# Kernel tuning notes

Measured on AMD Instinct MI355X. Metric: run time of the kernel, lower is better.

The kernel has to match this reference:

```python
import jax, jax.numpy as jnp
import numpy as np

N_QUBITS = 12
DIM = 2 ** N_QUBITS
N_RES_LAYERS = 3
N_HEADS = 2
N_ATTN_LAYERS = 2
SEQ_LEN = 64
HORIZON = 4
BATCH = 8
N_PARAMS = N_QUBITS * 2 * N_ATTN_LAYERS  # 48
FEAT = N_QUBITS * N_HEADS  # 24

# ---- static (numpy) precomputed gate structures (little-endian, qiskit convention) ----
_idx = np.arange(DIM)

def _cx_perm(c, t):
    # CNOT: flip target bit where control bit is 1 -> index permutation
    return np.where(((_idx >> c) & 1) == 1, _idx ^ (1 << t), _idx)

def _cz_phase(a, b):
    return (1.0 - 2.0 * (((_idx >> a) & 1) * ((_idx >> b) & 1))).astype(np.float32)

CX_LADDER = [jnp.asarray(_cx_perm(i, i + 1)) for i in range(N_QUBITS - 1)]
CX_RING = jnp.asarray(_cx_perm(N_QUBITS - 1, 0))
CX_LONG = jnp.asarray(_cx_perm(0, N_QUBITS - 1))
_CZ = []
for _layer in range(N_RES_LAYERS):
    _ph = np.ones(DIM, np.float32)
    for _i in range(_layer % 2, N_QUBITS - 1, 2):
        _ph *= _cz_phase(_i, _i + 1)
    _CZ.append(jnp.asarray(_ph))
# Qiskit Pauli label 'I'*i + 'Z' + 'I'*(n-i-1) acts on qubit n-1-i (big-endian labels)
Z_SIGNS = jnp.asarray(np.stack([
    (1.0 - 2.0 * ((_idx >> (N_QUBITS - 1 - i)) & 1)).astype(np.float32)
    for i in range(N_QUBITS)]))  # (n, DIM)


def _apply_1q(state, gate, q):
    # state: (..., DIM); gate: (2,2) or (...,2,2) broadcastable against leading dims
    hi = DIM >> (q + 1)
    lo = 1 << q
    s = state.reshape(state.shape[:-1] + (hi, 2, lo))
    out = jnp.einsum('...ij,...hjl->...hil', gate, s)
    return out.reshape(state.shape)


def _ry(theta):
    c = jnp.cos(theta / 2)
    s = jnp.sin(theta / 2)
    g = jnp.stack([jnp.stack([c, -s], -1), jnp.stack([s, c], -1)], -2)
    return g.astype(jnp.complex64)


def _rz(phi):
    em = jnp.exp(-0.5j * phi)
    ep = jnp.exp(0.5j * phi)
    z = jnp.zeros_like(em)
    return jnp.stack([jnp.stack([em, z], -1), jnp.stack([z, ep], -1)], -2)


def _u3(t, p, l):
    ct = jnp.cos(t / 2).astype(jnp.complex64)
    st = jnp.sin(t / 2).astype(jnp.complex64)
    return jnp.stack([jnp.stack([ct, -jnp.exp(1j * l) * st]),
                      jnp.stack([jnp.exp(1j * p) * st, jnp.exp(1j * (p + l)) * ct])])


def _encode_reservoir(x, res_params):
    # x: (B,T) normalized scalars -> batched statevectors (B,T,DIM)
    B, T = x.shape
    # H^{\otimes n} |0...0> = uniform superposition
    state = jnp.full((B, T, DIM), 1.0 / np.sqrt(DIM), jnp.complex64)
    for i in range(N_QUBITS):
        state = _apply_1q(state, _ry(x * np.pi * (i + 1) / N_QUBITS), i)
        state = _apply_1q(state, _rz(x * np.pi / (i + 1)), i)
    for p in CX_LADDER:
        state = state[..., p]
    state = state[..., CX_RING]
    # fixed random reservoir
    for layer in range(N_RES_LAYERS):
        for i in range(N_QUBITS):
            g = _u3(res_params[layer, i, 0], res_params[layer, i, 1], res_params[layer, i, 2])
            state = _apply_1q(state, g, i)
        state = state * _CZ[layer]
        state = state[..., CX_LONG]  # n > 2
    return state


def _project(state, params):
    # projection circuit: per layer RY/RZ on each qubit then CNOT ladder; then <Z_i>
    for layer in range(N_ATTN_LAYERS):
        for i in range(N_QUBITS):
            k = (layer * N_QUBITS + i) * 2
            state = _apply_1q(state, _ry(params[k]), i)
            state = _apply_1q(state, _rz(params[k + 1]), i)
        for p in CX_LADDER:
            state = state[..., p]
    probs = state.real ** 2 + state.imag ** 2  # (B,T,DIM)
    return jnp.einsum('btd,qd->btq', probs, Z_SIGNS)  # (B,T,n)


def setup_inputs() -> dict:
    key = jax.random.key(0)
    ks = jax.random.split(key, 6)
    sequence = jax.random.uniform(ks[0], (BATCH, SEQ_LEN), jnp.float32)
    res_params = jax.random.uniform(ks[1], (N_RES_LAYERS, N_QUBITS, 3), jnp.float32,
                                    minval=0.0, maxval=2.0 * np.pi)
    head_params = jax.random.uniform(ks[2], (N_HEADS, 3, N_PARAMS), jnp.float32,
                                     minval=0.0, maxval=2.0 * np.pi)
    W1 = jax.random.normal(ks[3], (FEAT, 2 * FEAT), jnp.float32) / np.sqrt(FEAT)
    b1 = jnp.zeros((2 * FEAT,), jnp.float32)
    W2 = jax.random.normal(ks[4], (2 * FEAT, HORIZON), jnp.float32) / np.sqrt(2 * FEAT)
    b2 = jnp.zeros((HORIZON,), jnp.float32)
    return {'sequence': sequence, 'res_params': res_params, 'head_params': head_params,
            'W1': W1, 'b1': b1, 'W2': W2, 'b2': b2}


def reference(sequence, res_params, head_params, W1, b1, W2, b2):
    states = _encode_reservoir(sequence, res_params)  # (B,T,DIM)
    T = sequence.shape[1]
    mask = jnp.triu(jnp.full((T, T), -1e9, jnp.float32), k=1)
    outs = []
    for h in range(N_HEADS):
        Q = _project(states, head_params[h, 0])
        K = _project(states, head_params[h, 1])
        V = _project(states, head_params[h, 2])
        scores = jnp.einsum('btd,bsd->bts', Q, K) / np.sqrt(N_QUBITS) + mask
        attn = jax.nn.softmax(scores, axis=-1)
        outs.append(jnp.einsum('bts,bsd->btd', attn, V))
    feats = jnp.concatenate(outs, -1)  # (B,T,FEAT)
    last = feats[:, -1, :]
    hdn = jax.nn.gelu(last @ W1 + b1, approximate=False)  # torch GELU default = exact erf
    pred = hdn @ W2 + b2  # (B, HORIZON)
    return pred
```

## Files before the change

### kernel.cpp

```cpp
#include <hip/hip_runtime.h>
#include <hip/hip_bf16.h>


#define PADDED 4224

__device__ __forceinline__ int PD(int j) { return j + (j >> 5); }

__device__ __forceinline__ int mapIdx(int j, int mode) {
  if (mode == 1) { int k = j ^ ((j >> 11) & 1); return k ^ ((k & 0x7FF) << 1); }
  if (mode == 2) { return j ^ ((j & 1) << 11); }
  if (mode == 3) { return j ^ ((j & 0x7FF) << 1); }
  return j;
}

template <int L>
__device__ __forceinline__ int layoutIdx(int tid, int r) {
  if constexpr (L == 0) return (tid << 4) | r;
  else if constexpr (L == 1) return ((tid & 0xF0) << 4) | (r << 4) | (tid & 15);
  else return (r << 8) | tid;
}

template <int L>
__device__ __forceinline__ void ldsRead16(const float* sR, const float* sI, int tid, int mode,
                                          float ar[16], float ai[16]) {
#pragma unroll
  for (int r = 0; r < 16; ++r) {
    int j = layoutIdx<L>(tid, r);
    int a = PD(mapIdx(j, mode));
    ar[r] = sR[a]; ai[r] = sI[a];
  }
}

template <int L>
__device__ __forceinline__ void ldsWrite16(float* sR, float* sI, int tid,
                                           const float ar[16], const float ai[16], int czmask) {
#pragma unroll
  for (int r = 0; r < 16; ++r) {
    int j = layoutIdx<L>(tid, r);
    float vr = ar[r], vi = ai[r];
    if (czmask) {
      float sg = (__popc((j & (j >> 1)) & czmask) & 1) ? -1.0f : 1.0f;
      vr *= sg; vi *= sg;
    }
    int a = PD(j);
    sR[a] = vr; sI[a] = vi;
  }
}

__device__ __forceinline__ void applyU34(float ar[16], float ai[16], const float (*ut)[8]) {
#pragma unroll
  for (int b = 0; b < 4; ++b) {
    const float* u = ut[b];
    float u00r = u[0];
    float u01r = u[2], u01i = u[3];
    float u10r = u[4], u10i = u[5], u11r = u[6], u11i = u[7];
#pragma unroll
    for (int m = 0; m < 8; ++m) {
      int p0 = ((m >> b) << (b + 1)) | (m & ((1 << b) - 1));
      int p1 = p0 | (1 << b);
      float x0r = ar[p0], x0i = ai[p0], x1r = ar[p1], x1i = ai[p1];
      ar[p0] = u00r * x0r + u01r * x1r - u01i * x1i;
      ai[p0] = u00r * x0i + u01r * x1i + u01i * x1r;
      ar[p1] = u10r * x0r - u10i * x0i + u11r * x1r - u11i * x1i;
      ai[p1] = u10r * x0i + u10i * x0r + u11r * x1i + u11i * x1r;
    }
  }
}

__device__ __forceinline__ void applyRyRz4(float ar[16], float ai[16], const float4* gt) {
#pragma unroll
  for (int b = 0; b < 4; ++b) {
    float4 g = gt[b];
    float c = g.x, s = g.y, zr = g.z, zi = g.w;
#pragma unroll
    for (int m = 0; m < 8; ++m) {
      int p0 = ((m >> b) << (b + 1)) | (m & ((1 << b) - 1));
      int p1 = p0 | (1 << b);
      float x0r = ar[p0], x0i = ai[p0], x1r = ar[p1], x1i = ai[p1];
      float n0r = c * x0r - s * x1r;
      float n0i = c * x0i - s * x1i;
      float wr  = s * x0r + c * x1r;
      float wi  = s * x0i + c * x1i;
      ar[p0] = n0r;              ai[p0] = n0i;
      ar[p1] = wr * zr - wi * zi; ai[p1] = wr * zi + wi * zr;
    }
  }
}

template <int L>
__device__ __forceinline__ void encPass(float* sR, float* sI, int tid, int mode,
                                        const float (*ut)[8], int czmask) {
  float ar[16], ai[16];
  ldsRead16<L>(sR, sI, tid, mode, ar, ai);
  if (mode != 0) __syncthreads();
  applyU34(ar, ai, ut);
  ldsWrite16<L>(sR, sI, tid, ar, ai, czmask);
  __syncthreads();
}

template <int L>
__device__ __forceinline__ void projPass(float* sR, float* sI, int tid, int mode, const float4* gt) {
  float ar[16], ai[16];
  ldsRead16<L>(sR, sI, tid, mode, ar, ai);
  if (mode != 0) __syncthreads();
  applyRyRz4(ar, ai, gt);
  ldsWrite16<L>(sR, sI, tid, ar, ai, 0);
  __syncthreads();
}

__device__ __forceinline__ void projFinal(const float* sR, const float* sI, int tid,
                                          const float4* gt, float feat[12]) {
  float ar[16], ai[16];
#pragma unroll
  for (int r = 0; r < 16; ++r) {
    int a = PD((r << 8) | tid);
    ar[r] = sR[a]; ai[r] = sI[a];
  }
  applyRyRz4(ar, ai, gt);
  float sp = 0.f, f0 = 0.f, f1 = 0.f, f2 = 0.f, f3 = 0.f;
  int pt = __popc(tid) & 1;
#pragma unroll
  for (int r = 0; r < 16; ++r) {
    float p = ar[r] * ar[r] + ai[r] * ai[r];
    sp += p;
    int tr = r ^ (r << 1); tr ^= (tr << 2);
    f0 += ((pt ^ ((tr >> 3) & 1)) ? -p : p);
    f1 += ((pt ^ ((tr >> 2) & 1)) ? -p : p);
    f2 += ((pt ^ ((tr >> 1) & 1)) ? -p : p);
    f3 += ((pt ^ (tr & 1)) ? -p : p);
  }
  feat[0] = f0; feat[1] = f1; feat[2] = f2; feat[3] = f3;
  int tt = tid ^ (tid << 1); tt ^= (tt << 2); tt ^= (tt << 4);
#pragma unroll
  for (int q = 4; q < 12; ++q)
    feat[q] = ((tt >> (11 - q)) & 1) ? -sp : sp;
}

__device__ __forceinline__ float waveReduce(float v) {
#pragma unroll
  for (int off = 32; off; off >>= 1) v += __shfl_xor(v, off, 64);
  return v;
}


__device__ __forceinline__ void buildQtab(float4* qtab, int tid, float x) {
  const float PI = 3.14159265358979323846f;
  const float RS2 = 0.70710678118654752440f;
  if (tid < 12) {
    int i = tid;
    float th = x * PI * (float)(i + 1) / 12.0f;
    float ph = x * PI / (float)(i + 1);
    float s, c;  sincosf(0.5f * th, &s, &c);
    float zi, zr; sincosf(0.5f * ph, &zi, &zr);
    float k0 = (c - s) * RS2, k1 = (c + s) * RS2;
    qtab[i] = make_float4(k0 * zr, -k0 * zi, k1 * zr, k1 * zi);
  }
}

__device__ __forceinline__ void buildUtab(float (*utab)[8], int tid, const float* resp) {
  if (tid >= 64 && tid < 100) {
    int i = tid - 64;
    const float* rp = resp + i * 3;
    float st, ct;  sincosf(0.5f * rp[0], &st, &ct);
    float sp2, cp; sincosf(rp[1], &sp2, &cp);
    float sl, cl;  sincosf(rp[2], &sl, &cl);
    float spl, cpl; sincosf(rp[1] + rp[2], &spl, &cpl);
    float* u = utab[i];
    u[0] = ct;       u[1] = 0.0f;
    u[2] = -cl * st; u[3] = -sl * st;
    u[4] = cp * st;  u[5] = sp2 * st;
    u[6] = cpl * ct; u[7] = spl * ct;
  }
}

__device__ __forceinline__ void initProduct(float* sRe, float* sIm, int tid, const float4* qtab) {
  float pr, pi;
  {
    float4 g = qtab[4];
    int sb = tid & 1;
    pr = sb ? g.z : g.x; pi = sb ? g.w : g.y;
  }
#pragma unroll
  for (int q = 5; q < 12; ++q) {
    float4 g = qtab[q];
    int sb = (tid >> (q - 4)) & 1;
    float fr = sb ? g.z : g.x, fi = sb ? g.w : g.y;
    float nr = pr * fr - pi * fi;
    pi = pr * fi + pi * fr; pr = nr;
  }
  float4 g0 = qtab[0], g1 = qtab[1], g2 = qtab[2], g3 = qtab[3];
  float c01r[4], c01i[4], c23r[4], c23i[4];
#pragma unroll
  for (int i2 = 0; i2 < 4; ++i2) {
    float f0r = (i2 & 1) ? g0.z : g0.x, f0i = (i2 & 1) ? g0.w : g0.y;
    float f1r = (i2 & 2) ? g1.z : g1.x, f1i = (i2 & 2) ? g1.w : g1.y;
    c01r[i2] = f0r * f1r - f0i * f1i; c01i[i2] = f0r * f1i + f0i * f1r;
    float f2r = (i2 & 1) ? g2.z : g2.x, f2i = (i2 & 1) ? g2.w : g2.y;
    float f3r = (i2 & 2) ? g3.z : g3.x, f3i = (i2 & 2) ? g3.w : g3.y;
    c23r[i2] = f2r * f3r - f2i * f3i; c23i[i2] = f2r * f3i + f2i * f3r;
  }
#pragma unroll
  for (int r = 0; r < 16; ++r) {
    float lr = c01r[r & 3] * c23r[r >> 2] - c01i[r & 3] * c23i[r >> 2];
    float li = c01r[r & 3] * c23i[r >> 2] + c01i[r & 3] * c23r[r >> 2];
    int a = PD((tid << 4) | r);
    sRe[a] = pr * lr - pi * li;
    sIm[a] = pr * li + pi * lr;
  }
}

__device__ __forceinline__ void buildPtab(float4* ptab, int tid, const float* hp) {
  if (tid < 24) {
    int k = tid * 2;
    float s, c;  sincosf(0.5f * hp[k], &s, &c);
    float zi, zr; sincosf(hp[k + 1], &zi, &zr);
    ptab[tid] = make_float4(c, s, zr, zi);
  }
}


__global__ __launch_bounds__(256, 2) void enc_kernel(
    const float* __restrict__ seq, const float* __restrict__ resp,
    float* __restrict__ wsStates) {
  __shared__ float sRe[PADDED], sIm[PADDED];
  __shared__ float4 qtab[12];
  __shared__ float utab[36][8];

  const int tid = threadIdx.x;
  const int blk = blockIdx.x;
  const float x = seq[blk];

  buildQtab(qtab, tid, x);
  buildUtab(utab, tid, resp);
  __syncthreads();

  initProduct(sRe, sIm, tid, qtab);
  __syncthreads();

  encPass<0>(sRe, sIm, tid, 1, &utab[0], 0);
  encPass<1>(sRe, sIm, tid, 0, &utab[4], 0);
  encPass<2>(sRe, sIm, tid, 0, &utab[8], 0x555);
  encPass<0>(sRe, sIm, tid, 2, &utab[12], 0);
  encPass<1>(sRe, sIm, tid, 0, &utab[16], 0);
  encPass<2>(sRe, sIm, tid, 0, &utab[20], 0x2AA);
  encPass<0>(sRe, sIm, tid, 2, &utab[24], 0);
  encPass<1>(sRe, sIm, tid, 0, &utab[28], 0);

  {
    float ar[16], ai[16];
    ldsRead16<2>(sRe, sIm, tid, 0, ar, ai);
    applyU34(ar, ai, &utab[32]);
    float* gR = wsStates + (size_t)blk * 8192;
    float* gI = gR + 4096;
#pragma unroll
    for (int r = 0; r < 16; ++r) {
      int j = (r << 8) | tid;
      float sg = (__popc((j & (j >> 1)) & 0x555) & 1) ? -1.0f : 1.0f;
      int g = j ^ ((j & 1) << 11);
      gR[g] = sg * ar[r];
      gI[g] = sg * ai[r];
    }
  }
}

__global__ __launch_bounds__(256, 4) void proj_kernel(
    const float* __restrict__ wsStates, const float* __restrict__ hparams,
    float* __restrict__ featBase) {
  __shared__ float sRe[PADDED], sIm[PADDED];
  __shared__ float4 ptab[24];
  __shared__ float red[4][12];

  const int tid = threadIdx.x;
  const int bid = blockIdx.x;
  int h, which, s;
  if (bid < 2048) { s = bid >> 2; int pp = bid & 3; h = pp >> 1; which = 1 + (pp & 1); }
  else            { int i = bid - 2048; h = i & 1; s = (((i >> 1) << 6) | 63); which = 0; }
  const int b = s >> 6, t = s & 63;

  buildPtab(ptab, tid, hparams + (h * 3 + which) * 48);

  float ar[16], ai[16];
  const float4* pR = (const float4*)(wsStates + (size_t)s * 8192 + (tid << 4));
  const float4* pI = (const float4*)(wsStates + (size_t)s * 8192 + 4096 + (tid << 4));
#pragma unroll
  for (int k = 0; k < 4; ++k) {
    float4 vr = pR[k], vi = pI[k];
    ar[4 * k] = vr.x; ar[4 * k + 1] = vr.y; ar[4 * k + 2] = vr.z; ar[4 * k + 3] = vr.w;
    ai[4 * k] = vi.x; ai[4 * k + 1] = vi.y; ai[4 * k + 2] = vi.z; ai[4 * k + 3] = vi.w;
  }
  __syncthreads();

  applyRyRz4(ar, ai, &ptab[0]);
  ldsWrite16<0>(sRe, sIm, tid, ar, ai, 0);
  __syncthreads();

  projPass<1>(sRe, sIm, tid, 0, &ptab[4]);
  projPass<2>(sRe, sIm, tid, 0, &ptab[8]);
  projPass<0>(sRe, sIm, tid, 3, &ptab[12]);
  projPass<1>(sRe, sIm, tid, 0, &ptab[16]);

  float feat[12];
  projFinal(sRe, sIm, tid, &ptab[20], feat);
#pragma unroll
  for (int q = 0; q < 12; ++q) feat[q] = waveReduce(feat[q]);
  int wid = tid >> 6;
  if ((tid & 63) == 0) {
#pragma unroll
    for (int q = 0; q < 12; ++q) red[wid][q] = feat[q];
  }
  __syncthreads();
  if (tid < 12) {
    float v = red[0][tid] + red[1][tid] + red[2][tid] + red[3][tid];
    float* dst;
    if (which == 1)      dst = featBase + (((h << 3) + b) * 64 + t) * 12;
    else if (which == 2) dst = featBase + 12288 + (((h << 3) + b) * 64 + t) * 12;
    else                 dst = featBase + 24576 + ((h << 3) + b) * 12;
    dst[tid] = v;
  }
}


__global__ __launch_bounds__(256, 2) void qstates_mono(
    const float* __restrict__ seq, const float* __restrict__ resp,
    const float* __restrict__ hparams, float* __restrict__ featBase) {
  __shared__ float sRe[PADDED], sIm[PADDED];
  __shared__ float4 qtab[12];
  __shared__ float utab[36][8];
  __shared__ float4 ptab[24];
  __shared__ float red[4][12];

  const int tid = threadIdx.x;
  const int blk = blockIdx.x;
  const int b = blk >> 6;
  const int t = blk & 63;
  const float x = seq[blk];

  buildQtab(qtab, tid, x);
  buildUtab(utab, tid, resp);
  __syncthreads();
  initProduct(sRe, sIm, tid, qtab);
  __syncthreads();

  for (int l = 0; l < 3; ++l) {
    int czm = (l & 1) ? 0x2AA : 0x555;
    encPass<0>(sRe, sIm, tid, (l == 0) ? 1 : 2, &utab[l * 12], 0);
    encPass<1>(sRe, sIm, tid, 0, &utab[l * 12 + 4], 0);
    encPass<2>(sRe, sIm, tid, 0, &utab[l * 12 + 8], czm);
  }

  float encR[16], encI[16];
#pragma unroll
  for (int r = 0; r < 16; ++r) {
    int j = (tid << 4) | r;
    int a = PD(j ^ ((j & 1) << 11));
    encR[r] = sRe[a]; encI[r] = sIm[a];
  }

  const int nproj = (t == 63) ? 6 : 4;
  for (int pj = 0; pj < nproj; ++pj) {
    int h, which;
    if (pj < 4) { h = pj >> 1; which = (pj & 1) ? 2 : 1; }
    else        { h = pj - 4;  which = 0; }
    buildPtab(ptab, tid, hparams + (h * 3 + which) * 48);
    __syncthreads();

    float ar[16], ai[16];
#pragma unroll
    for (int r = 0; r < 16; ++r) { ar[r] = encR[r]; ai[r] = encI[r]; }
    applyRyRz4(ar, ai, &ptab[0]);
    ldsWrite16<0>(sRe, sIm, tid, ar, ai, 0);
    __syncthreads();
    projPass<1>(sRe, sIm, tid, 0, &ptab[4]);
    projPass<2>(sRe, sIm, tid, 0, &ptab[8]);
    projPass<0>(sRe, sIm, tid, 3, &ptab[12]);
    projPass<1>(sRe, sIm, tid, 0, &ptab[16]);

    float feat[12];
    projFinal(sRe, sIm, tid, &ptab[20], feat);
#pragma unroll
    for (int q = 0; q < 12; ++q) feat[q] = waveReduce(feat[q]);
    int wid = tid >> 6;
    if ((tid & 63) == 0) {
#pragma unroll
      for (int q = 0; q < 12; ++q) red[wid][q] = feat[q];
    }
    __syncthreads();
    if (tid < 12) {
      float v = red[0][tid] + red[1][tid] + red[2][tid] + red[3][tid];
      float* dst;
      if (which == 1)      dst = featBase + (((h << 3) + b) * 64 + t) * 12;
      else if (which == 2) dst = featBase + 12288 + (((h << 3) + b) * 64 + t) * 12;
      else                 dst = featBase + 24576 + ((h << 3) + b) * 12;
      dst[tid] = v;
    }
    __syncthreads();
  }
}


__global__ __launch_bounds__(64) void qhead_kernel(
    const float* __restrict__ featBase,
    const float* __restrict__ W1, const float* __restrict__ b1,
    const float* __restrict__ W2, const float* __restrict__ b2,
    float* __restrict__ out) {
  __shared__ float feats[24];
  __shared__ float hdn[48];
  const int b = blockIdx.x;
  const int lane = threadIdx.x;
  const float* Kf = featBase;
  const float* Vf = featBase + 12288;
  const float* Qf = featBase + 24576;
  for (int h = 0; h < 2; ++h) {
    const float* q  = Qf + ((h << 3) + b) * 12;
    const float* kr = Kf + ((((h << 3) + b) << 6) + lane) * 12;
    float dot = 0.f;
#pragma unroll
    for (int d = 0; d < 12; ++d) dot += q[d] * kr[d];
    dot *= 0.288675134594812882f;
    float mx = dot;
#pragma unroll
    for (int off = 32; off; off >>= 1) mx = fmaxf(mx, __shfl_xor(mx, off, 64));
    float e = expf(dot - mx);
    float se = e;
#pragma unroll
    for (int off = 32; off; off >>= 1) se += __shfl_xor(se, off, 64);
    float a = e / se;
    const float* vr = Vf + ((((h << 3) + b) << 6) + lane) * 12;
#pragma unroll
    for (int d = 0; d < 12; ++d) {
      float v = a * vr[d];
#pragma unroll
      for (int off = 32; off; off >>= 1) v += __shfl_xor(v, off, 64);
      if (lane == 0) feats[h * 12 + d] = v;
    }
  }
  __syncthreads();
  if (lane < 48) {
    float acc = b1[lane];
#pragma unroll
    for (int f = 0; f < 24; ++f) acc += feats[f] * W1[f * 48 + lane];
    hdn[lane] = 0.5f * acc * (1.0f + erff(acc * 0.70710678118654752440f));
  }
  __syncthreads();
  if (lane < 4) {
    float acc = b2[lane];
#pragma unroll
    for (int k = 0; k < 48; ++k) acc += hdn[k] * W2[k * 4 + lane];
    out[(b << 2) | lane] = acc;
  }
}

extern "C" void kernel_launch(void* const* d_in, const int* in_sizes, int n_in,
                              void* d_out, int out_size, void* d_ws, size_t ws_size,
                              hipStream_t stream) {
  const float* seq     = (const float*)d_in[0];
  const float* resp    = (const float*)d_in[1];
  const float* hparams = (const float*)d_in[2];
  const float* W1      = (const float*)d_in[3];
  const float* b1      = (const float*)d_in[4];
  const float* W2      = (const float*)d_in[5];
  const float* b2      = (const float*)d_in[6];
  float* out = (float*)d_out;
  float* ws  = (float*)d_ws;

  const size_t needSplit = ((size_t)512 * 8192 + 24768) * sizeof(float);
  if (ws_size >= needSplit) {
    float* wsStates = ws;
    float* featBase = ws + (size_t)512 * 8192;
    hipLaunchKernelGGL(enc_kernel, dim3(512), dim3(256), 0, stream, seq, resp, wsStates);
    hipLaunchKernelGGL(proj_kernel, dim3(2064), dim3(256), 0, stream, wsStates, hparams, featBase);
    hipLaunchKernelGGL(qhead_kernel, dim3(8), dim3(64), 0, stream, featBase, W1, b1, W2, b2, out);
  } else {
    hipLaunchKernelGGL(qstates_mono, dim3(512), dim3(256), 0, stream, seq, resp, hparams, ws);
    hipLaunchKernelGGL(qhead_kernel, dim3(8), dim3(64), 0, stream, ws, W1, b1, W2, b2, out);
  }
}
```

Measured before the change: 147.9 us.

## Restructure encoder and projection kernels to single-wave blocks with 64 amplitudes per lane

Replaces the 256-thread encoder and projection kernels with 64-thread (single wavefront) versions. Each lane now holds 64 complex amplitudes, so six qubits are applied per register pass, which needs fewer LDS transposes, and the LDS layout uses an XOR swizzle instead of padding. Gate tables are precomputed once in a new prep kernel instead of in every block. In exchange, register use per lane grows sharply and occupancy is lower, and an extra kernel launch is added.

```diff
diff --git a/kernel.cpp b/kernel.cpp
--- a/kernel.cpp
+++ b/kernel.cpp
@@ -2,35 +2,311 @@
 #include <hip/hip_bf16.h>
 
 
+#define N_STATE_F (512 * 8192)
+#define WS_FEAT   N_STATE_F
+#define WS_PTAB   (WS_FEAT + 24768)
+#define WS_UTAB   (WS_PTAB + 576)
+#define WS_TOTAL  (WS_UTAB + 288)
+
+#define SWZ(j) ((j) ^ (((j) >> 6) & 63))
+
+__device__ __forceinline__ float xorf(float a, unsigned m) {
+  return __int_as_float(__float_as_int(a) ^ (int)m);
+}
+
+template <int MODE>
+__device__ __forceinline__ int mapIdxT(int j) {
+  if constexpr (MODE == 1) { int k = j ^ ((j >> 11) & 1); return k ^ ((k & 0x7FF) << 1); }
+  else if constexpr (MODE == 2) return j ^ ((j & 1) << 11);
+  else if constexpr (MODE == 3) return j ^ ((j & 0x7FF) << 1);
+  else return j;
+}
+
+
+__device__ __forceinline__ void wA64(float* sR, float* sI, int l,
+                                     const float (&ar)[64], const float (&ai)[64]) {
+#pragma unroll
+  for (int r = 0; r < 64; ++r) {
+    int idx = SWZ((l << 6) | r);
+    sR[idx] = ar[r]; sI[idx] = ai[r];
+  }
+}
+__device__ __forceinline__ void wB64(float* sR, float* sI, int l,
+                                     const float (&ar)[64], const float (&ai)[64]) {
+#pragma unroll
+  for (int r = 0; r < 64; ++r) {
+    int idx = SWZ((r << 6) | l);
+    sR[idx] = ar[r]; sI[idx] = ai[r];
+  }
+}
+template <int MODE>
+__device__ __forceinline__ void rA64(const float* sR, const float* sI, int l,
+                                     float (&ar)[64], float (&ai)[64]) {
+#pragma unroll
+  for (int r = 0; r < 64; ++r) {
+    int idx = SWZ(mapIdxT<MODE>((l << 6) | r));
+    ar[r] = sR[idx]; ai[r] = sI[idx];
+  }
+}
+template <int MODE>
+__device__ __forceinline__ void rB64(const float* sR, const float* sI, int l,
+                                     float (&ar)[64], float (&ai)[64]) {
+#pragma unroll
+  for (int r = 0; r < 64; ++r) {
+    int idx = SWZ(mapIdxT<MODE>((r << 6) | l));
+    ar[r] = sR[idx]; ai[r] = sI[idx];
+  }
+}
+
+template <int B>
+__device__ __forceinline__ void u3g(float (&ar)[64], float (&ai)[64], const float* u) {
+  float u00 = u[0], u01r = u[2], u01i = u[3], u10r = u[4], u10i = u[5], u11r = u[6], u11i = u[7];
+#pragma unroll
+  for (int m = 0; m < 32; ++m) {
+    int p0 = ((m >> B) << (B + 1)) | (m & ((1 << B) - 1));
+    int p1 = p0 | (1 << B);
+    float x0r = ar[p0], x0i = ai[p0], x1r = ar[p1], x1i = ai[p1];
+    ar[p0] = u00 * x0r + u01r * x1r - u01i * x1i;
+    ai[p0] = u00 * x0i + u01r * x1i + u01i * x1r;
+    ar[p1] = u10r * x0r - u10i * x0i + u11r * x1r - u11i * x1i;
+    ai[p1] = u10r * x0i + u10i * x0r + u11r * x1i + u11i * x1r;
+  }
+}
+__device__ __forceinline__ void u3Group6(float (&ar)[64], float (&ai)[64], const float* ub) {
+  u3g<0>(ar, ai, ub);       u3g<1>(ar, ai, ub + 8);   u3g<2>(ar, ai, ub + 16);
+  u3g<3>(ar, ai, ub + 24);  u3g<4>(ar, ai, ub + 32);  u3g<5>(ar, ai, ub + 40);
+}
+
+template <int B>
+__device__ __forceinline__ void ryrzg(float (&ar)[64], float (&ai)[64], float4 g) {
+  float c = g.x, s = g.y, zr = g.z, zi = g.w;
+#pragma unroll
+  for (int m = 0; m < 32; ++m) {
+    int p0 = ((m >> B) << (B + 1)) | (m & ((1 << B) - 1));
+    int p1 = p0 | (1 << B);
+    float x0r = ar[p0], x0i = ai[p0], x1r = ar[p1], x1i = ai[p1];
+    float n0r = c * x0r - s * x1r;
+    float n0i = c * x0i - s * x1i;
+    float wr  = s * x0r + c * x1r;
+    float wi  = s * x0i + c * x1i;
+    ar[p0] = n0r;               ai[p0] = n0i;
+    ar[p1] = wr * zr - wi * zi; ai[p1] = wr * zi + wi * zr;
+  }
+}
+__device__ __forceinline__ void ryrzGroup6(float (&ar)[64], float (&ai)[64], const float4* gt) {
+  ryrzg<0>(ar, ai, gt[0]); ryrzg<1>(ar, ai, gt[1]); ryrzg<2>(ar, ai, gt[2]);
+  ryrzg<3>(ar, ai, gt[3]); ryrzg<4>(ar, ai, gt[4]); ryrzg<5>(ar, ai, gt[5]);
+}
+
+template <int TYPE>
+__device__ __forceinline__ void czB64(float (&ar)[64], float (&ai)[64], int l) {
+  if constexpr (TYPE == 0) {
+    unsigned mL = (unsigned)(__popc((l & (l >> 1)) & 0x15) & 1) << 31;
+#pragma unroll
+    for (int r = 0; r < 64; ++r) {
+      unsigned m = mL ^ ((unsigned)(__popc((r & (r >> 1)) & 0x15) & 1) << 31);
+      ar[r] = xorf(ar[r], m); ai[r] = xorf(ai[r], m);
+    }
+  } else {
+    unsigned mE = (unsigned)(__popc((l & (l >> 1)) & 0xA) & 1) << 31;
+    unsigned mO = mE ^ ((unsigned)((l >> 5) & 1) << 31);
+#pragma unroll
+    for (int r = 0; r < 64; ++r) {
+      unsigned m = ((r & 1) ? mO : mE) ^ ((unsigned)(__popc((r & (r >> 1)) & 0xA) & 1) << 31);
+      ar[r] = xorf(ar[r], m); ai[r] = xorf(ai[r], m);
+    }
+  }
+}
+
+__global__ void prep_kernel(const float* __restrict__ hparams,
+                            const float* __restrict__ resp, float* __restrict__ ws) {
+  int t = threadIdx.x;
+  float4* ptab = (float4*)(ws + WS_PTAB);
+  for (int idx = t; idx < 144; idx += 256) {
+    int pj = idx / 24, k = idx % 24;
+    const float* hp = hparams + pj * 48;
+    float s, c;  sincosf(0.5f * hp[2 * k], &s, &c);
+    float zi, zr; sincosf(hp[2 * k + 1], &zi, &zr);
+    ptab[idx] = make_float4(c, s, zr, zi);
+  }
+  if (t < 36) {
+    const float* rp = resp + t * 3;
+    float st, ct;  sincosf(0.5f * rp[0], &st, &ct);
+    float sp2, cp; sincosf(rp[1], &sp2, &cp);
+    float sl, cl;  sincosf(rp[2], &sl, &cl);
+    float spl, cpl; sincosf(rp[1] + rp[2], &spl, &cpl);
+    float* u = ws + WS_UTAB + t * 8;
+    u[0] = ct;       u[1] = 0.0f;
+    u[2] = -cl * st; u[3] = -sl * st;
+    u[4] = cp * st;  u[5] = sp2 * st;
+    u[6] = cpl * ct; u[7] = spl * ct;
+  }
+}
+
+__global__ __launch_bounds__(64) void enc64_kernel(
+    const float* __restrict__ seq, const float* __restrict__ utabG,
+    float* __restrict__ wsStates) {
+  __shared__ float sRe[4096], sIm[4096];
+  __shared__ float4 qtab[12];
+  const int l = threadIdx.x;
+  const int s = blockIdx.x;
+  const float x = seq[s];
+  const float PI = 3.14159265358979323846f;
+  const float RS2 = 0.70710678118654752440f;
+  if (l < 12) {
+    float th = x * PI * (float)(l + 1) / 12.0f;
+    float ph = x * PI / (float)(l + 1);
+    float sn, cs;  sincosf(0.5f * th, &sn, &cs);
+    float zi, zr;  sincosf(0.5f * ph, &zi, &zr);
+    float k0 = (cs - sn) * RS2, k1 = (cs + sn) * RS2;
+    qtab[l] = make_float4(k0 * zr, -k0 * zi, k1 * zr, k1 * zi);
+  }
+  __syncthreads();
+
+  float ar[64], ai[64];
+  float pr, pi;
+  { float4 g = qtab[0]; pr = (l & 1) ? g.z : g.x; pi = (l & 1) ? g.w : g.y; }
+#pragma unroll
+  for (int q = 1; q < 6; ++q) {
+    float4 g = qtab[q];
+    int bb = (l >> q) & 1;
+    float fr = bb ? g.z : g.x, fi = bb ? g.w : g.y;
+    float nr = pr * fr - pi * fi; pi = pr * fi + pi * fr; pr = nr;
+  }
+  ar[0] = pr; ai[0] = pi;
+#pragma unroll
+  for (int k = 0; k < 6; ++k) {
+    float4 g = qtab[6 + k];
+#pragma unroll
+    for (int m = 0; m < (1 << k); ++m) {
+      float xr = ar[m], xi = ai[m];
+      ar[m | (1 << k)] = xr * g.z - xi * g.w;
+      ai[m | (1 << k)] = xr * g.w + xi * g.z;
+      ar[m] = xr * g.x - xi * g.y;
+      ai[m] = xr * g.y + xi * g.x;
+    }
+  }
+
+  wB64(sRe, sIm, l, ar, ai); __syncthreads();
+  rA64<1>(sRe, sIm, l, ar, ai);
+  u3Group6(ar, ai, utabG + 0);
+  __syncthreads(); wA64(sRe, sIm, l, ar, ai); __syncthreads();
+  rB64<0>(sRe, sIm, l, ar, ai);
+  u3Group6(ar, ai, utabG + 6 * 8);
+  czB64<0>(ar, ai, l);
+  __syncthreads(); wB64(sRe, sIm, l, ar, ai); __syncthreads();
+  rA64<2>(sRe, sIm, l, ar, ai);
+  u3Group6(ar, ai, utabG + 12 * 8);
+  __syncthreads(); wA64(sRe, sIm, l, ar, ai); __syncthreads();
+  rB64<0>(sRe, sIm, l, ar, ai);
+  u3Group6(ar, ai, utabG + 18 * 8);
+  czB64<1>(ar, ai, l);
+  __syncthreads(); wB64(sRe, sIm, l, ar, ai); __syncthreads();
+  rA64<2>(sRe, sIm, l, ar, ai);
+  u3Group6(ar, ai, utabG + 24 * 8);
+  __syncthreads(); wA64(sRe, sIm, l, ar, ai); __syncthreads();
+  rB64<0>(sRe, sIm, l, ar, ai);
+  u3Group6(ar, ai, utabG + 30 * 8);
+  czB64<0>(ar, ai, l);
+
+  float* gR = wsStates + (size_t)s * 8192;
+  float* gI = gR + 4096;
+  int lf5 = (l & 1) << 5;
+#pragma unroll
+  for (int r = 0; r < 64; ++r) {
+    int g = ((r ^ lf5) << 6) | l;
+    gR[g] = ar[r]; gI[g] = ai[r];
+  }
+}
+
+__global__ __launch_bounds__(64) void proj64_kernel(
+    const float* __restrict__ wsStates, const float* __restrict__ ptabG,
+    float* __restrict__ featBase) {
+  __shared__ float sRe[4096], sIm[4096];
+  const int l = threadIdx.x;
+  const int bid = blockIdx.x;
+  int h, which, s;
+  if (bid < 2048) { s = bid >> 2; int pp = bid & 3; h = pp >> 1; which = 1 + (pp & 1); }
+  else            { int i = bid - 2048; h = i & 1; s = (((i >> 1) << 6) | 63); which = 0; }
+  const int b = s >> 6, t = s & 63;
+  const float4* gt = (const float4*)ptabG + (h * 3 + which) * 24;
+  const float* stR = wsStates + (size_t)s * 8192;
+  const float* stI = stR + 4096;
+
+  float ar[64], ai[64];
+#pragma unroll
+  for (int r = 0; r < 64; ++r) {
+    ar[r] = stR[(r << 6) | l];
+    ai[r] = stI[(r << 6) | l];
+  }
+  ryrzGroup6(ar, ai, gt + 6);
+  __syncthreads(); wB64(sRe, sIm, l, ar, ai); __syncthreads();
+  rA64<0>(sRe, sIm, l, ar, ai);
+  ryrzGroup6(ar, ai, gt + 0);
+  __syncthreads(); wA64(sRe, sIm, l, ar, ai); __syncthreads();
+  rB64<3>(sRe, sIm, l, ar, ai);
+  ryrzGroup6(ar, ai, gt + 18);
+  __syncthreads(); wB64(sRe, sIm, l, ar, ai); __syncthreads();
+  rA64<0>(sRe, sIm, l, ar, ai);
+  ryrzGroup6(ar, ai, gt + 12);
+
+  float acc0 = 0, a7 = 0, a8 = 0, a9 = 0, a10 = 0, a11 = 0;
+#pragma unroll
+  for (int r = 0; r < 64; ++r) {
+    float p = ar[r] * ar[r] + ai[r] * ai[r];
+    if (__popc(r & 63) & 1) acc0 -= p; else acc0 += p;
+    if (__popc(r & 31) & 1) a7 -= p; else a7 += p;
+    if (__popc(r & 15) & 1) a8 -= p; else a8 += p;
+    if (__popc(r & 7) & 1)  a9 -= p; else a9 += p;
+    if (__popc(r & 3) & 1)  a10 -= p; else a10 += p;
+    if (__popc(r & 1) & 1)  a11 -= p; else a11 += p;
+  }
+  float f[12];
+  f[0] = xorf(acc0, (unsigned)(__popc(l & 63) & 1) << 31);
+  f[1] = xorf(acc0, (unsigned)(__popc(l & 31) & 1) << 31);
+  f[2] = xorf(acc0, (unsigned)(__popc(l & 15) & 1) << 31);
+  f[3] = xorf(acc0, (unsigned)(__popc(l & 7) & 1) << 31);
+  f[4] = xorf(acc0, (unsigned)(__popc(l & 3) & 1) << 31);
+  f[5] = xorf(acc0, (unsigned)(__popc(l & 1) & 1) << 31);
+  f[6] = acc0; f[7] = a7; f[8] = a8; f[9] = a9; f[10] = a10; f[11] = a11;
+#pragma unroll
+  for (int q = 0; q < 12; ++q) {
+#pragma unroll
+    for (int off = 32; off; off >>= 1) f[q] += __shfl_xor(f[q], off, 64);
+  }
+  if (l == 0) {
+    float* dst;
+    if (which == 1)      dst = featBase + (((h << 3) + b) * 64 + t) * 12;
+    else if (which == 2) dst = featBase + 12288 + (((h << 3) + b) * 64 + t) * 12;
+    else                 dst = featBase + 24576 + ((h << 3) + b) * 12;
+#pragma unroll
+    for (int q = 0; q < 12; ++q) dst[q] = f[q];
+  }
+}
+
 #define PADDED 4224
-
 __device__ __forceinline__ int PD(int j) { return j + (j >> 5); }
-
 __device__ __forceinline__ int mapIdx(int j, int mode) {
   if (mode == 1) { int k = j ^ ((j >> 11) & 1); return k ^ ((k & 0x7FF) << 1); }
   if (mode == 2) { return j ^ ((j & 1) << 11); }
   if (mode == 3) { return j ^ ((j & 0x7FF) << 1); }
   return j;
 }
-
 template <int L>
 __device__ __forceinline__ int layoutIdx(int tid, int r) {
   if constexpr (L == 0) return (tid << 4) | r;
   else if constexpr (L == 1) return ((tid & 0xF0) << 4) | (r << 4) | (tid & 15);
   else return (r << 8) | tid;
 }
-
 template <int L>
 __device__ __forceinline__ void ldsRead16(const float* sR, const float* sI, int tid, int mode,
                                           float ar[16], float ai[16]) {
 #pragma unroll
   for (int r = 0; r < 16; ++r) {
-    int j = layoutIdx<L>(tid, r);
-    int a = PD(mapIdx(j, mode));
+    int a = PD(mapIdx(layoutIdx<L>(tid, r), mode));
     ar[r] = sR[a]; ai[r] = sI[a];
   }
 }
-
 template <int L>
 __device__ __forceinline__ void ldsWrite16(float* sR, float* sI, int tid,
                                            const float ar[16], const float ai[16], int czmask) {
@@ -46,13 +322,11 @@
     sR[a] = vr; sI[a] = vi;
   }
 }
-
 __device__ __forceinline__ void applyU34(float ar[16], float ai[16], const float (*ut)[8]) {
 #pragma unroll
   for (int b = 0; b < 4; ++b) {
     const float* u = ut[b];
-    float u00r = u[0];
-    float u01r = u[2], u01i = u[3];
+    float u00r = u[0], u01r = u[2], u01i = u[3];
     float u10r = u[4], u10i = u[5], u11r = u[6], u11i = u[7];
 #pragma unroll
     for (int m = 0; m < 8; ++m) {
@@ -66,7 +340,6 @@
     }
   }
 }
-
 __device__ __forceinline__ void applyRyRz4(float ar[16], float ai[16], const float4* gt) {
 #pragma unroll
   for (int b = 0; b < 4; ++b) {
@@ -81,12 +354,11 @@
       float n0i = c * x0i - s * x1i;
       float wr  = s * x0r + c * x1r;
       float wi  = s * x0i + c * x1i;
-      ar[p0] = n0r;              ai[p0] = n0i;
+      ar[p0] = n0r;               ai[p0] = n0i;
       ar[p1] = wr * zr - wi * zi; ai[p1] = wr * zi + wi * zr;
     }
   }
 }
-
 template <int L>
 __device__ __forceinline__ void encPass(float* sR, float* sI, int tid, int mode,
                                         const float (*ut)[8], int czmask) {
@@ -97,7 +369,6 @@
   ldsWrite16<L>(sR, sI, tid, ar, ai, czmask);
   __syncthreads();
 }
-
 template <int L>
 __device__ __forceinline__ void projPass(float* sR, float* sI, int tid, int mode, const float4* gt) {
   float ar[16], ai[16];
@@ -107,7 +378,6 @@
   ldsWrite16<L>(sR, sI, tid, ar, ai, 0);
   __syncthreads();
 }
-
 __device__ __forceinline__ void projFinal(const float* sR, const float* sI, int tid,
                                           const float4* gt, float feat[12]) {
   float ar[16], ai[16];
@@ -135,28 +405,23 @@
   for (int q = 4; q < 12; ++q)
     feat[q] = ((tt >> (11 - q)) & 1) ? -sp : sp;
 }
-
 __device__ __forceinline__ float waveReduce(float v) {
 #pragma unroll
   for (int off = 32; off; off >>= 1) v += __shfl_xor(v, off, 64);
   return v;
 }
-
-
 __device__ __forceinline__ void buildQtab(float4* qtab, int tid, float x) {
   const float PI = 3.14159265358979323846f;
   const float RS2 = 0.70710678118654752440f;
   if (tid < 12) {
-    int i = tid;
-    float th = x * PI * (float)(i + 1) / 12.0f;
-    float ph = x * PI / (float)(i + 1);
+    float th = x * PI * (float)(tid + 1) / 12.0f;
+    float ph = x * PI / (float)(tid + 1);
     float s, c;  sincosf(0.5f * th, &s, &c);
     float zi, zr; sincosf(0.5f * ph, &zi, &zr);
     float k0 = (c - s) * RS2, k1 = (c + s) * RS2;
-    qtab[i] = make_float4(k0 * zr, -k0 * zi, k1 * zr, k1 * zi);
-  }
-}
-
+    qtab[tid] = make_float4(k0 * zr, -k0 * zi, k1 * zr, k1 * zi);
+  }
+}
 __device__ __forceinline__ void buildUtab(float (*utab)[8], int tid, const float* resp) {
   if (tid >= 64 && tid < 100) {
     int i = tid - 64;
@@ -172,14 +437,9 @@
     u[6] = cpl * ct; u[7] = spl * ct;
   }
 }
-
 __device__ __forceinline__ void initProduct(float* sRe, float* sIm, int tid, const float4* qtab) {
   float pr, pi;
-  {
-    float4 g = qtab[4];
-    int sb = tid & 1;
-    pr = sb ? g.z : g.x; pi = sb ? g.w : g.y;
-  }
+  { float4 g = qtab[4]; int sb = tid & 1; pr = sb ? g.z : g.x; pi = sb ? g.w : g.y; }
 #pragma unroll
   for (int q = 5; q < 12; ++q) {
     float4 g = qtab[q];
@@ -208,7 +468,6 @@
     sIm[a] = pr * li + pi * lr;
   }
 }
-
 __device__ __forceinline__ void buildPtab(float4* ptab, int tid, const float* hp) {
   if (tid < 24) {
     int k = tid * 2;
@@ -217,109 +476,6 @@
     ptab[tid] = make_float4(c, s, zr, zi);
   }
 }
-
-
-__global__ __launch_bounds__(256, 2) void enc_kernel(
-    const float* __restrict__ seq, const float* __restrict__ resp,
-    float* __restrict__ wsStates) {
-  __shared__ float sRe[PADDED], sIm[PADDED];
-  __shared__ float4 qtab[12];
-  __shared__ float utab[36][8];
-
-  const int tid = threadIdx.x;
-  const int blk = blockIdx.x;
-  const float x = seq[blk];
-
-  buildQtab(qtab, tid, x);
-  buildUtab(utab, tid, resp);
-  __syncthreads();
-
-  initProduct(sRe, sIm, tid, qtab);
-  __syncthreads();
-
-  encPass<0>(sRe, sIm, tid, 1, &utab[0], 0);
-  encPass<1>(sRe, sIm, tid, 0, &utab[4], 0);
-  encPass<2>(sRe, sIm, tid, 0, &utab[8], 0x555);
-  encPass<0>(sRe, sIm, tid, 2, &utab[12], 0);
-  encPass<1>(sRe, sIm, tid, 0, &utab[16], 0);
-  encPass<2>(sRe, sIm, tid, 0, &utab[20], 0x2AA);
-  encPass<0>(sRe, sIm, tid, 2, &utab[24], 0);
-  encPass<1>(sRe, sIm, tid, 0, &utab[28], 0);
-
-  {
-    float ar[16], ai[16];
-    ldsRead16<2>(sRe, sIm, tid, 0, ar, ai);
-    applyU34(ar, ai, &utab[32]);
-    float* gR = wsStates + (size_t)blk * 8192;
-    float* gI = gR + 4096;
-#pragma unroll
-    for (int r = 0; r < 16; ++r) {
-      int j = (r << 8) | tid;
-      float sg = (__popc((j & (j >> 1)) & 0x555) & 1) ? -1.0f : 1.0f;
-      int g = j ^ ((j & 1) << 11);
-      gR[g] = sg * ar[r];
-      gI[g] = sg * ai[r];
-    }
-  }
-}
-
-__global__ __launch_bounds__(256, 4) void proj_kernel(
-    const float* __restrict__ wsStates, const float* __restrict__ hparams,
-    float* __restrict__ featBase) {
-  __shared__ float sRe[PADDED], sIm[PADDED];
-  __shared__ float4 ptab[24];
-  __shared__ float red[4][12];
-
-  const int tid = threadIdx.x;
-  const int bid = blockIdx.x;
-  int h, which, s;
-  if (bid < 2048) { s = bid >> 2; int pp = bid & 3; h = pp >> 1; which = 1 + (pp & 1); }
-  else            { int i = bid - 2048; h = i & 1; s = (((i >> 1) << 6) | 63); which = 0; }
-  const int b = s >> 6, t = s & 63;
-
-  buildPtab(ptab, tid, hparams + (h * 3 + which) * 48);
-
-  float ar[16], ai[16];
-  const float4* pR = (const float4*)(wsStates + (size_t)s * 8192 + (tid << 4));
-  const float4* pI = (const float4*)(wsStates + (size_t)s * 8192 + 4096 + (tid << 4));
-#pragma unroll
-  for (int k = 0; k < 4; ++k) {
-    float4 vr = pR[k], vi = pI[k];
-    ar[4 * k] = vr.x; ar[4 * k + 1] = vr.y; ar[4 * k + 2] = vr.z; ar[4 * k + 3] = vr.w;
-    ai[4 * k] = vi.x; ai[4 * k + 1] = vi.y; ai[4 * k + 2] = vi.z; ai[4 * k + 3] = vi.w;
-  }
-  __syncthreads();
-
-  applyRyRz4(ar, ai, &ptab[0]);
-  ldsWrite16<0>(sRe, sIm, tid, ar, ai, 0);
-  __syncthreads();
-
-  projPass<1>(sRe, sIm, tid, 0, &ptab[4]);
-  projPass<2>(sRe, sIm, tid, 0, &ptab[8]);
-  projPass<0>(sRe, sIm, tid, 3, &ptab[12]);
-  projPass<1>(sRe, sIm, tid, 0, &ptab[16]);
-
-  float feat[12];
-  projFinal(sRe, sIm, tid, &ptab[20], feat);
-#pragma unroll
-  for (int q = 0; q < 12; ++q) feat[q] = waveReduce(feat[q]);
-  int wid = tid >> 6;
-  if ((tid & 63) == 0) {
-#pragma unroll
-    for (int q = 0; q < 12; ++q) red[wid][q] = feat[q];
-  }
-  __syncthreads();
-  if (tid < 12) {
-    float v = red[0][tid] + red[1][tid] + red[2][tid] + red[3][tid];
-    float* dst;
-    if (which == 1)      dst = featBase + (((h << 3) + b) * 64 + t) * 12;
-    else if (which == 2) dst = featBase + 12288 + (((h << 3) + b) * 64 + t) * 12;
-    else                 dst = featBase + 24576 + ((h << 3) + b) * 12;
-    dst[tid] = v;
-  }
-}
-
-
 __global__ __launch_bounds__(256, 2) void qstates_mono(
     const float* __restrict__ seq, const float* __restrict__ resp,
     const float* __restrict__ hparams, float* __restrict__ featBase) {
@@ -328,26 +484,21 @@
   __shared__ float utab[36][8];
   __shared__ float4 ptab[24];
   __shared__ float red[4][12];
-
   const int tid = threadIdx.x;
   const int blk = blockIdx.x;
-  const int b = blk >> 6;
-  const int t = blk & 63;
+  const int b = blk >> 6, t = blk & 63;
   const float x = seq[blk];
-
   buildQtab(qtab, tid, x);
   buildUtab(utab, tid, resp);
   __syncthreads();
   initProduct(sRe, sIm, tid, qtab);
   __syncthreads();
-
   for (int l = 0; l < 3; ++l) {
     int czm = (l & 1) ? 0x2AA : 0x555;
     encPass<0>(sRe, sIm, tid, (l == 0) ? 1 : 2, &utab[l * 12], 0);
     encPass<1>(sRe, sIm, tid, 0, &utab[l * 12 + 4], 0);
     encPass<2>(sRe, sIm, tid, 0, &utab[l * 12 + 8], czm);
   }
-
   float encR[16], encI[16];
 #pragma unroll
   for (int r = 0; r < 16; ++r) {
@@ -355,7 +506,6 @@
     int a = PD(j ^ ((j & 1) << 11));
     encR[r] = sRe[a]; encI[r] = sIm[a];
   }
-
   const int nproj = (t == 63) ? 6 : 4;
   for (int pj = 0; pj < nproj; ++pj) {
     int h, which;
@@ -363,7 +513,6 @@
     else        { h = pj - 4;  which = 0; }
     buildPtab(ptab, tid, hparams + (h * 3 + which) * 48);
     __syncthreads();
-
     float ar[16], ai[16];
 #pragma unroll
     for (int r = 0; r < 16; ++r) { ar[r] = encR[r]; ai[r] = encI[r]; }
@@ -374,7 +523,6 @@
     projPass<2>(sRe, sIm, tid, 0, &ptab[8]);
     projPass<0>(sRe, sIm, tid, 3, &ptab[12]);
     projPass<1>(sRe, sIm, tid, 0, &ptab[16]);
-
     float feat[12];
     projFinal(sRe, sIm, tid, &ptab[20], feat);
 #pragma unroll
@@ -396,7 +544,6 @@
     __syncthreads();
   }
 }
-
 
 __global__ __launch_bounds__(64) void qhead_kernel(
     const float* __restrict__ featBase,
@@ -463,12 +610,15 @@
   float* out = (float*)d_out;
   float* ws  = (float*)d_ws;
 
-  const size_t needSplit = ((size_t)512 * 8192 + 24768) * sizeof(float);
+  const size_t needSplit = (size_t)WS_TOTAL * sizeof(float);
   if (ws_size >= needSplit) {
     float* wsStates = ws;
-    float* featBase = ws + (size_t)512 * 8192;
-    hipLaunchKernelGGL(enc_kernel, dim3(512), dim3(256), 0, stream, seq, resp, wsStates);
-    hipLaunchKernelGGL(proj_kernel, dim3(2064), dim3(256), 0, stream, wsStates, hparams, featBase);
+    float* featBase = ws + WS_FEAT;
+    float* ptabG    = ws + WS_PTAB;
+    float* utabG    = ws + WS_UTAB;
+    hipLaunchKernelGGL(prep_kernel, dim3(1), dim3(256), 0, stream, hparams, resp, ws);
+    hipLaunchKernelGGL(enc64_kernel, dim3(512), dim3(64), 0, stream, seq, utabG, wsStates);
+    hipLaunchKernelGGL(proj64_kernel, dim3(2064), dim3(64), 0, stream, wsStates, ptabG, featBase);
     hipLaunchKernelGGL(qhead_kernel, dim3(8), dim3(64), 0, stream, featBase, W1, b1, W2, b2, out);
   } else {
     hipLaunchKernelGGL(qstates_mono, dim3(512), dim3(256), 0, stream, seq, resp, hparams, ws);
```

After: 216.3 us. 1.46x slower.
